# Performance work log

Measured on AMD Instinct MI355X. Metric: run time of the kernel, lower is better.

Reference implementation:

```python
import jax, jax.numpy as jnp
import numpy as np

N, F_IN, D_OUT, H = 8192, 512, 64, 8
ALPHA = 0.2
NEG_INF = jnp.float32(-9e15)


def setup_inputs() -> dict:
    key = jax.random.key(0)
    k1, k2, k3, k4, k5 = jax.random.split(key, 5)
    x = jax.random.normal(k1, (N, F_IN), dtype=jnp.float32)
    # sparse-ish binary adjacency (avg degree ~33) with self-loops, stored dense
    adj = (jax.random.uniform(k2, (N, N)) < 0.004).astype(jnp.float32)
    adj = jnp.maximum(adj, jnp.eye(N, dtype=jnp.float32))
    W = jax.random.normal(k3, (H, F_IN, D_OUT), dtype=jnp.float32) * 0.05
    a1 = jax.random.normal(k4, (H, D_OUT), dtype=jnp.float32) * 0.05
    a2 = jax.random.normal(k5, (H, D_OUT), dtype=jnp.float32) * 0.05
    return {"x": x, "adj": adj, "W": W, "a1": a1, "a2": a2}


def reference(x, adj, W, a1, a2):
    mask = adj > 0
    outputs = []
    for h in range(H):  # fixed small head count (matches original per-head loop)
        Wh = x @ W[h]                      # [N, D]
        f1 = Wh @ a1[h]                    # [N]
        f2 = Wh @ a2[h]                    # [N]
        e = jax.nn.leaky_relu(f1[:, None] + f2[None, :], ALPHA)  # [N, N]
        att = jnp.where(mask, e, NEG_INF)
        att = jax.nn.softmax(att, axis=1)  # dropout omitted (eval mode)
        outputs.append(att @ Wh)           # [N, D]
    return jnp.concatenate(outputs, axis=1)  # [N, H*D]
```

## Files before the change

kernel.cpp:

```cpp
#include <hip/hip_runtime.h>
#include <hip/hip_bf16.h>
#include <cstdint>

#define N_NODES 8192
#define F_IN    512
#define D_O     64
#define H_N     8
#define NOUT    512
#define MAXD    128

#define BM 64
#define BN 128
#define BK 64

typedef __attribute__((ext_vector_type(8))) short short8;
typedef __attribute__((ext_vector_type(4))) float f32x4;
typedef __attribute__((ext_vector_type(4))) unsigned int uintv4;

static __device__ __forceinline__ ushort f2bf(float f) {
  union { float f; uint32_t u; } v; v.f = f;
  uint32_t r = v.u + 0x7FFFu + ((v.u >> 16) & 1u);
  return (ushort)(r >> 16);
}
static __device__ __forceinline__ float bf2f(ushort u) {
  union { uint32_t u; float f; } v; v.u = ((uint32_t)u) << 16;
  return v.f;
}

__global__ __launch_bounds__(256) void convert(const float* __restrict__ x,
                                               const float* __restrict__ W,
                                               ushort* __restrict__ xb,
                                               ushort* __restrict__ Wt) {
  __shared__ float Ws[64][65];
  const int b = blockIdx.x, t = threadIdx.x;
  if (b < 2048) {
    const int gid = b * 256 + t;
    #pragma unroll
    for (int it = 0; it < 2; ++it) {
      const int q = gid + it * 524288;
      const float4 v = ((const float4*)x)[q];
      ushort4 u;
      u.x = f2bf(v.x); u.y = f2bf(v.y); u.z = f2bf(v.z); u.w = f2bf(v.w);
      ((ushort4*)xb)[q] = u;
    }
  } else {
    const int bb = b - 2048;
    const int h = bb >> 3, kt = bb & 7;
    const int d = t & 63, krg = (t >> 6) * 16;
    const float* src = &W[((size_t)h * F_IN + kt * 64 + krg) * D_O + d];
    #pragma unroll
    for (int q = 0; q < 16; ++q)
      Ws[krg + q][d] = src[(size_t)q * D_O];
    __syncthreads();
    const int d0 = t >> 2, kq = (t & 3) * 16;
    ushort* dst = &Wt[(size_t)h * D_O * F_IN + (size_t)d0 * F_IN + kt * 64 + kq];
    #pragma unroll
    for (int q = 0; q < 16; ++q)
      dst[q] = f2bf(Ws[kq + q][d0]);
  }
}

__global__ __launch_bounds__(256) void scan_gemm(const uint32_t* __restrict__ adj,
                                                 const ushort* __restrict__ xb,
                                                 const ushort* __restrict__ Wt,
                                                 const float* __restrict__ a1,
                                                 const float* __restrict__ a2,
                                                 ushort* __restrict__ Whb,
                                                 float* __restrict__ f1,
                                                 float* __restrict__ f2,
                                                 ushort* __restrict__ nbr_g,
                                                 int* __restrict__ deg_g) {
  __shared__ ushort As[BM][BK + 8];
  __shared__ ushort Bs[BN][BK + 8];
  __shared__ int wsum[4];

  const int id   = blockIdx.x;
  const int tid  = threadIdx.x;
  const int lane = tid & 63;
  const int wv   = tid >> 6;

  if (id < 512) {
    const int wr = wv >> 1, wc = wv & 1;
    const int r0 = (id >> 2) * BM;
    const int c0 = (id & 3) * BN;
    const int lm = lane & 15;
    const int lg = lane >> 4;

    f32x4 acc[2][4];
    #pragma unroll
    for (int m2 = 0; m2 < 2; ++m2)
      #pragma unroll
      for (int n2 = 0; n2 < 4; ++n2)
        acc[m2][n2] = (f32x4){0.f, 0.f, 0.f, 0.f};

    for (int k0 = 0; k0 < F_IN; k0 += BK) {
      __syncthreads();
      #pragma unroll
      for (int p = 0; p < 2; ++p) {
        const int e = p * 256 + tid;
        const int row = e >> 3, ck = (e & 7) * 8;
        *(short8*)&As[row][ck] = *(const short8*)&xb[(size_t)(r0 + row) * F_IN + k0 + ck];
      }
      #pragma unroll
      for (int p = 0; p < 4; ++p) {
        const int e = p * 256 + tid;
        const int row = e >> 3, ck = (e & 7) * 8;
        *(short8*)&Bs[row][ck] = *(const short8*)&Wt[(size_t)(c0 + row) * F_IN + k0 + ck];
      }
      __syncthreads();

      #pragma unroll
      for (int kk = 0; kk < 2; ++kk) {
        const int koff = kk * 32 + lg * 8;
        short8 af[2], bf[4];
        #pragma unroll
        for (int m2 = 0; m2 < 2; ++m2)
          af[m2] = *(const short8*)&As[wr * 32 + m2 * 16 + lm][koff];
        #pragma unroll
        for (int n2 = 0; n2 < 4; ++n2)
          bf[n2] = *(const short8*)&Bs[wc * 64 + n2 * 16 + lm][koff];
        #pragma unroll
        for (int m2 = 0; m2 < 2; ++m2)
          #pragma unroll
          for (int n2 = 0; n2 < 4; ++n2)
            acc[m2][n2] = __builtin_amdgcn_mfma_f32_16x16x32_bf16(af[m2], bf[n2], acc[m2][n2], 0, 0, 0);
      }
    }

    const int head = (c0 >> 6) + wc;
    float a1v[4], a2v[4];
    #pragma unroll
    for (int n2 = 0; n2 < 4; ++n2) {
      a1v[n2] = a1[head * D_O + n2 * 16 + lm];
      a2v[n2] = a2[head * D_O + n2 * 16 + lm];
    }
    #pragma unroll
    for (int m2 = 0; m2 < 2; ++m2) {
      #pragma unroll
      for (int r = 0; r < 4; ++r) {
        const int row = r0 + wr * 32 + m2 * 16 + lg * 4 + r;
        float p1 = 0.f, p2 = 0.f;
        #pragma unroll
        for (int n2 = 0; n2 < 4; ++n2) {
          const float v = acc[m2][n2][r];
          p1 += v * a1v[n2];
          p2 += v * a2v[n2];
          Whb[(size_t)row * NOUT + c0 + wc * 64 + n2 * 16 + lm] = f2bf(v);
        }
        #pragma unroll
        for (int o = 1; o < 16; o <<= 1) {
          p1 += __shfl_xor(p1, o);
          p2 += __shfl_xor(p2, o);
        }
        if (lm == 0) {
          f1[(size_t)row * H_N + head] = p1;
          f2[(size_t)row * H_N + head] = p2;
        }
      }
    }
  } else {
    const int i = id - 512;
    const uint32_t* arow = adj + (size_t)i * N_NODES;
    uint32_t bits = 0;
    #pragma unroll
    for (int u = 0; u < 8; ++u) {
      const uintv4 a = __builtin_nontemporal_load(
          (const uintv4*)&arow[(u * 256 + tid) * 4]);
      if (a.x) bits |= 1u << (u * 4 + 0);
      if (a.y) bits |= 1u << (u * 4 + 1);
      if (a.z) bits |= 1u << (u * 4 + 2);
      if (a.w) bits |= 1u << (u * 4 + 3);
    }
    const int cnt = __popc(bits);
    int v = cnt;
    #pragma unroll
    for (int o = 1; o < 64; o <<= 1) {
      int u = __shfl_up(v, o);
      if (lane >= o) v += u;
    }
    if (lane == 63) wsum[wv] = v;
    __syncthreads();
    int base = 0, total = 0;
    #pragma unroll
    for (int ww = 0; ww < 4; ++ww) {
      int s = wsum[ww];
      if (ww < wv) base += s;
      total += s;
    }
    int off = base + v - cnt;
    #pragma unroll
    for (int u = 0; u < 8; ++u)
      #pragma unroll
      for (int bq = 0; bq < 4; ++bq)
        if (bits & (1u << (u * 4 + bq))) {
          if (off < MAXD) nbr_g[(size_t)i * MAXD + off] = (ushort)((u * 256 + tid) * 4 + bq);
          ++off;
        }
    if (tid == 0) deg_g[i] = min(total, MAXD);
  }
}

__global__ __launch_bounds__(256) void gat_panel(const ushort* __restrict__ nbr_g,
                                                 const int* __restrict__ deg_g,
                                                 const ushort* __restrict__ Whb,
                                                 const float* __restrict__ f1,
                                                 const float* __restrict__ f2,
                                                 float* __restrict__ out) {
  const int bid = blockIdx.x;
  const int xcd = bid & 7;
  const int P   = xcd >> 1;
  const int w   = threadIdx.x >> 6;
  const int i   = (bid >> 3) * 8 + (xcd & 1) * 4 + w;
  const int t   = threadIdx.x & 63;

  __shared__ int   nbr[4][MAXD];
  __shared__ float ps[4][MAXD][2];

  const int deg = deg_g[i];
  if (t < deg)      nbr[w][t]      = nbr_g[(size_t)i * MAXD + t];
  if (t + 64 < deg) nbr[w][t + 64] = nbr_g[(size_t)i * MAXD + t + 64];

  const int h = t >> 5;
  const int l = t & 31;
  const float f1v = f1[(size_t)i * H_N + 2 * P + h];
  float s = 0.f;
  for (int n = l; n < deg; n += 32) {
    const float2 v = *(const float2*)&f2[(size_t)nbr[w][n] * H_N + 2 * P];
    float e = f1v + (h ? v.y : v.x);
    e = e > 0.f ? e : 0.2f * e;
    e = __expf(e);
    ps[w][n][h] = e;
    s += e;
  }
  #pragma unroll
  for (int o = 16; o; o >>= 1) s += __shfl_xor(s, o);
  const float inv = 1.0f / s;

  const int colbase = P * 128 + t * 2;
  float a0 = 0.f, a1c = 0.f;
  #pragma unroll 8
  for (int n = 0; n < deg; ++n) {
    const float pv = ps[w][n][h];
    const ushort2 u = *(const ushort2*)&Whb[(size_t)nbr[w][n] * NOUT + colbase];
    a0  += pv * bf2f(u.x);
    a1c += pv * bf2f(u.y);
  }
  float2 o2; o2.x = a0 * inv; o2.y = a1c * inv;
  *(float2*)&out[(size_t)i * NOUT + colbase] = o2;
}

extern "C" void kernel_launch(void* const* d_in, const int* in_sizes, int n_in,
                              void* d_out, int out_size, void* d_ws, size_t ws_size,
                              hipStream_t stream) {
  const float* x   = (const float*)d_in[0];
  const float* adj = (const float*)d_in[1];
  const float* W   = (const float*)d_in[2];
  const float* a1  = (const float*)d_in[3];
  const float* a2  = (const float*)d_in[4];
  float* out = (float*)d_out;

  ushort* Whb = (ushort*)d_ws;
  ushort* xb  = Whb + (size_t)N_NODES * NOUT;
  ushort* Wt  = xb + (size_t)N_NODES * F_IN;
  float*  f1  = (float*)(Wt + (size_t)H_N * D_O * F_IN);
  float*  f2  = f1 + (size_t)N_NODES * H_N;
  ushort* nbr_g = (ushort*)(f2 + (size_t)N_NODES * H_N);
  int*    deg_g = (int*)(nbr_g + (size_t)N_NODES * MAXD);

  hipLaunchKernelGGL(convert, dim3(2112), dim3(256), 0, stream, x, W, xb, Wt);
  hipLaunchKernelGGL(scan_gemm, dim3(512 + N_NODES), dim3(256), 0, stream,
                     (const uint32_t*)adj, xb, Wt, a1, a2, Whb, f1, f2, nbr_g, deg_g);
  hipLaunchKernelGGL(gat_panel, dim3(N_NODES), dim3(256), 0, stream,
                     nbr_g, deg_g, Whb, f1, f2, out);
}
```

Before: 89.78 us.

## Store Wh per-head contiguously and map gat_panel blocks to one head each

```diff
diff --git a/kernel.cpp b/kernel.cpp
--- a/kernel.cpp
+++ b/kernel.cpp
@@ -65,7 +65,7 @@
                                                  const ushort* __restrict__ Wt,
                                                  const float* __restrict__ a1,
                                                  const float* __restrict__ a2,
-                                                 ushort* __restrict__ Whb,
+                                                 ushort* __restrict__ Whbp,
                                                  float* __restrict__ f1,
                                                  float* __restrict__ f2,
                                                  ushort* __restrict__ nbr_g,
@@ -145,7 +145,7 @@
           const float v = acc[m2][n2][r];
           p1 += v * a1v[n2];
           p2 += v * a2v[n2];
-          Whb[(size_t)row * NOUT + c0 + wc * 64 + n2 * 16 + lm] = f2bf(v);
+          Whbp[((size_t)head * N_NODES + row) * D_O + n2 * 16 + lm] = f2bf(v);
         }
         #pragma unroll
         for (int o = 1; o < 16; o <<= 1) {
@@ -202,51 +202,58 @@
 
 __global__ __launch_bounds__(256) void gat_panel(const ushort* __restrict__ nbr_g,
                                                  const int* __restrict__ deg_g,
-                                                 const ushort* __restrict__ Whb,
+                                                 const ushort* __restrict__ Whbp,
                                                  const float* __restrict__ f1,
                                                  const float* __restrict__ f2,
                                                  float* __restrict__ out) {
   const int bid = blockIdx.x;
-  const int xcd = bid & 7;
-  const int P   = xcd >> 1;
+  const int P   = bid & 7;
   const int w   = threadIdx.x >> 6;
-  const int i   = (bid >> 3) * 8 + (xcd & 1) * 4 + w;
+  const int i   = (bid >> 3) * 4 + w;
   const int t   = threadIdx.x & 63;
 
   __shared__ int   nbr[4][MAXD];
-  __shared__ float ps[4][MAXD][2];
+  __shared__ float ps[4][MAXD];
 
   const int deg = deg_g[i];
   if (t < deg)      nbr[w][t]      = nbr_g[(size_t)i * MAXD + t];
   if (t + 64 < deg) nbr[w][t + 64] = nbr_g[(size_t)i * MAXD + t + 64];
 
-  const int h = t >> 5;
-  const int l = t & 31;
-  const float f1v = f1[(size_t)i * H_N + 2 * P + h];
-  float s = 0.f;
-  for (int n = l; n < deg; n += 32) {
-    const float2 v = *(const float2*)&f2[(size_t)nbr[w][n] * H_N + 2 * P];
-    float e = f1v + (h ? v.y : v.x);
+  const float f1v = f1[(size_t)i * H_N + P];
+  float e0 = 0.f, e1 = 0.f;
+  if (t < deg) {
+    float e = f1v + f2[(size_t)nbr[w][t] * H_N + P];
     e = e > 0.f ? e : 0.2f * e;
-    e = __expf(e);
-    ps[w][n][h] = e;
-    s += e;
-  }
+    e0 = __expf(e);
+    ps[w][t] = e0;
+  }
+  if (t + 64 < deg) {
+    float e = f1v + f2[(size_t)nbr[w][t + 64] * H_N + P];
+    e = e > 0.f ? e : 0.2f * e;
+    e1 = __expf(e);
+    ps[w][t + 64] = e1;
+  }
+  float s = e0 + e1;
   #pragma unroll
-  for (int o = 16; o; o >>= 1) s += __shfl_xor(s, o);
+  for (int o = 32; o; o >>= 1) s += __shfl_xor(s, o);
   const float inv = 1.0f / s;
 
-  const int colbase = P * 128 + t * 2;
+  const int q  = t >> 5;
+  const int c2 = (t & 31) * 2;
   float a0 = 0.f, a1c = 0.f;
   #pragma unroll 8
-  for (int n = 0; n < deg; ++n) {
-    const float pv = ps[w][n][h];
-    const ushort2 u = *(const ushort2*)&Whb[(size_t)nbr[w][n] * NOUT + colbase];
+  for (int n = q; n < deg; n += 2) {
+    const float pv = ps[w][n];
+    const ushort2 u = *(const ushort2*)&Whbp[((size_t)P * N_NODES + nbr[w][n]) * D_O + c2];
     a0  += pv * bf2f(u.x);
     a1c += pv * bf2f(u.y);
   }
-  float2 o2; o2.x = a0 * inv; o2.y = a1c * inv;
-  *(float2*)&out[(size_t)i * NOUT + colbase] = o2;
+  a0  += __shfl_xor(a0, 32);
+  a1c += __shfl_xor(a1c, 32);
+  if (t < 32) {
+    float2 o2; o2.x = a0 * inv; o2.y = a1c * inv;
+    *(float2*)&out[(size_t)i * NOUT + P * D_O + c2] = o2;
+  }
 }
 
 extern "C" void kernel_launch(void* const* d_in, const int* in_sizes, int n_in,
@@ -259,8 +266,8 @@
   const float* a2  = (const float*)d_in[4];
   float* out = (float*)d_out;
 
-  ushort* Whb = (ushort*)d_ws;
-  ushort* xb  = Whb + (size_t)N_NODES * NOUT;
+  ushort* Whbp = (ushort*)d_ws;
+  ushort* xb  = Whbp + (size_t)N_NODES * NOUT;
   ushort* Wt  = xb + (size_t)N_NODES * F_IN;
   float*  f1  = (float*)(Wt + (size_t)H_N * D_O * F_IN);
   float*  f2  = f1 + (size_t)N_NODES * H_N;
@@ -269,7 +276,7 @@
 
   hipLaunchKernelGGL(convert, dim3(2112), dim3(256), 0, stream, x, W, xb, Wt);
   hipLaunchKernelGGL(scan_gemm, dim3(512 + N_NODES), dim3(256), 0, stream,
-                     (const uint32_t*)adj, xb, Wt, a1, a2, Whb, f1, f2, nbr_g, deg_g);
-  hipLaunchKernelGGL(gat_panel, dim3(N_NODES), dim3(256), 0, stream,
-                     nbr_g, deg_g, Whb, f1, f2, out);
-}
+                     (const uint32_t*)adj, xb, Wt, a1, a2, Whbp, f1, f2, nbr_g, deg_g);
+  hipLaunchKernelGGL(gat_panel, dim3(8 * N_NODES / 4), dim3(256), 0, stream,
+                     nbr_g, deg_g, Whbp, f1, f2, out);
+}
```

After: 97.93 us. 9.1% more time.
